# Performance work log

Hardware: AMD Instinct MI355X
Metric: run time of the kernel (lower is better)

## Reference

```python
import jax, jax.numpy as jnp
import numpy as np

D = 2048        # input_size / model dim
H = 2816        # hidden_size per expert (GLU -> w1 has 2*H rows)
E = 8           # num_experts
M = 4096        # tokens (batch*seq)


def setup_inputs() -> dict:
    key = jax.random.key(0)
    k1, k2, k3, k4, k5 = jax.random.split(key, 5)
    x = jax.random.normal(k1, (M, D), dtype=jnp.float32)
    # ParallelExperts init: uniform(-1/fan_in_dim, 1/fan_in_dim); scale kept simple here
    w1 = jax.random.uniform(k2, (E, 2 * H, D), dtype=jnp.float32, minval=-1.0, maxval=1.0) / (2 * H)
    w2 = jax.random.uniform(k3, (E, D, H), dtype=jnp.float32, minval=-1.0, maxval=1.0) / D
    router_w = jax.random.normal(k4, (E, D), dtype=jnp.float32) * (1.0 / np.sqrt(D))
    bias = jnp.zeros((D,), dtype=jnp.float32)
    return {"x": x, "w1": w1, "w2": w2, "router_w": router_w, "bias": bias, "top_k": 2}


def _moe_forward(x, w1, w2, router_w, bias, top_k):
    # Router: logits -> softmax (fp32) -> top-k -> renormalize (fused_moe semantics)
    logits = x @ router_w.T                                # [M, E]
    probs = jax.nn.softmax(logits.astype(jnp.float32), axis=-1)
    topk_w, topk_ids = jax.lax.top_k(probs, top_k)         # [M, k]
    topk_w = topk_w / jnp.sum(topk_w, axis=-1, keepdims=True)
    # Dense combine weights [M, E]: gate weight if expert selected, else 0
    m = x.shape[0]
    combine = jnp.zeros((m, w1.shape[0]), dtype=x.dtype)
    combine = combine.at[jnp.arange(m)[:, None], topk_ids].add(topk_w.astype(x.dtype))
    # Grouped expert GEMMs, expressed as a loop over the small fixed expert set.
    # Contribution of expert e is masked by combine[:, e] (zero for unrouted tokens).
    y = jnp.zeros_like(x)
    hdim = w2.shape[2]
    for e in range(w1.shape[0]):
        g = x @ w1[e].T                                    # [M, 2H]
        h = jax.nn.silu(g[:, :hdim]) * g[:, hdim:]          # silu_and_mul (GLU)
        y = y + combine[:, e:e + 1] * (h @ w2[e].T)         # [M, D]
    return y + bias


def reference(x, w1, w2, router_w, bias, top_k):
    return _moe_forward(x, w1, w2, router_w, bias, top_k)
```

## Files before the change

kernel.cpp:

```cpp
#include <hip/hip_runtime.h>
#include <hip/hip_bf16.h>
#include <stdint.h>

#define M_TOK 4096
#define DDIM  2048
#define HDIM  2816
#define NEXP  8
#define PMAX  9216
#define MAXTILES 72
#define NT1   44
#define NT2   16
#define KT1   32
#define KT2   44

typedef __attribute__((ext_vector_type(8))) short short8;
typedef __attribute__((ext_vector_type(4))) float f32x4;

#define GLD16(g, l) __builtin_amdgcn_global_load_lds(                              \
    (const __attribute__((address_space(1))) unsigned int*)(g),                    \
    (__attribute__((address_space(3))) unsigned int*)(l), 16, 0, 0)

__device__ __forceinline__ unsigned short f2bf(float f) {
  unsigned int u = __float_as_uint(f);
  u += 0x7fffu + ((u >> 16) & 1u);
  return (unsigned short)(u >> 16);
}

__device__ __forceinline__ short8 ldsfrag(const unsigned short* base, int r, int kk) {
  int b = (r << 7) + (kk << 1);
  b ^= (r & 7) << 4;
  return *(const short8*)((const char*)base + b);
}

__global__ void cvt_bf16_k(const float4* __restrict__ in, ushort4* __restrict__ out, int n4) {
  int stride = gridDim.x * blockDim.x;
  for (int i = blockIdx.x * blockDim.x + threadIdx.x; i < n4; i += stride) {
    float4 v = in[i];
    ushort4 o;
    o.x = f2bf(v.x); o.y = f2bf(v.y); o.z = f2bf(v.z); o.w = f2bf(v.w);
    out[i] = o;
  }
}

__global__ void init_k(int* __restrict__ tok, int* __restrict__ counts, int* __restrict__ cursors) {
  int i = blockIdx.x * blockDim.x + threadIdx.x;
  if (i < PMAX) tok[i] = -1;
  if (i < NEXP) { counts[i] = 0; cursors[i] = 0; }
}

__global__ __launch_bounds__(256) void router_k(const float* __restrict__ x,
                                                const float* __restrict__ rw,
                                                float* __restrict__ wgt,
                                                int* __restrict__ eid,
                                                int* __restrict__ counts) {
  int lane = threadIdx.x & 63;
  int wv = threadIdx.x >> 6;
  int t = blockIdx.x * 4 + wv;
  const float* xr = x + (size_t)t * DDIM;
  float acc[NEXP];
#pragma unroll
  for (int e = 0; e < NEXP; ++e) acc[e] = 0.f;
  for (int j = 0; j < DDIM / 64; ++j) {
    float xv = xr[lane + j * 64];
#pragma unroll
    for (int e = 0; e < NEXP; ++e) acc[e] += xv * rw[e * DDIM + lane + j * 64];
  }
#pragma unroll
  for (int e = 0; e < NEXP; ++e) {
#pragma unroll
    for (int s = 32; s > 0; s >>= 1) acc[e] += __shfl_xor(acc[e], s, 64);
  }
  if (lane == 0) {
    float mx = acc[0];
#pragma unroll
    for (int e = 1; e < NEXP; ++e) mx = fmaxf(mx, acc[e]);
    float p[NEXP];
#pragma unroll
    for (int e = 0; e < NEXP; ++e) p[e] = expf(acc[e] - mx);
    int e0 = 0; float p0 = p[0];
#pragma unroll
    for (int e = 1; e < NEXP; ++e) if (p[e] > p0) { p0 = p[e]; e0 = e; }
    int e1 = -1; float p1 = -1.f;
#pragma unroll
    for (int e = 0; e < NEXP; ++e) if (e != e0 && p[e] > p1) { p1 = p[e]; e1 = e; }
    float s = p0 + p1;
    wgt[2 * t] = p0 / s; wgt[2 * t + 1] = p1 / s;
    eid[2 * t] = e0;     eid[2 * t + 1] = e1;
    atomicAdd(&counts[e0], 1);
    atomicAdd(&counts[e1], 1);
  }
}

__global__ void offsets_k(const int* __restrict__ counts, int* __restrict__ offs,
                          int* __restrict__ tile2exp, int* __restrict__ tilerow,
                          int* __restrict__ ntiles) {
  if (threadIdx.x == 0 && blockIdx.x == 0) {
    int o = 0, nt = 0;
    for (int e = 0; e < NEXP; ++e) {
      offs[e] = o;
      int c = counts[e];
      int pt = (c + 127) >> 7;
      for (int i = 0; i < pt; ++i) { tile2exp[nt] = e; tilerow[nt] = o + i * 128; ++nt; }
      o += pt << 7;
    }
    offs[NEXP] = o;
    ntiles[0] = nt;
  }
}

__global__ void scatter_k(const int* __restrict__ eid, const int* __restrict__ offs,
                          int* __restrict__ cursors, int* __restrict__ tok,
                          int* __restrict__ slot) {
  int t = blockIdx.x * blockDim.x + threadIdx.x;
  if (t >= M_TOK) return;
#pragma unroll
  for (int k = 0; k < 2; ++k) {
    int e = eid[2 * t + k];
    int p = offs[e] + atomicAdd(&cursors[e], 1);
    tok[p] = t;
    slot[2 * t + k] = p;
  }
}

__global__ __launch_bounds__(256) void gemm1_k(const unsigned short* __restrict__ xb,
                                               const unsigned short* __restrict__ w1b,
                                               const int* __restrict__ tok,
                                               const int* __restrict__ tile2exp,
                                               const int* __restrict__ tilerow,
                                               const int* __restrict__ ntiles,
                                               unsigned short* __restrict__ h) {
  __shared__ unsigned short lA[128 * 64];
  __shared__ unsigned short lBg[64 * 64];
  __shared__ unsigned short lBu[64 * 64];
  int mt = blockIdx.x;
  if (mt >= ntiles[0]) return;
  int e  = tile2exp[mt];
  int r0 = tilerow[mt];
  int n0 = blockIdx.y * 64;
  int tid = threadIdx.x;
  int lane = tid & 63, wv = tid >> 6;

  int srow = tid >> 3;
  int g16 = (tid & 7) ^ (srow & 7);
  const char* aptr[4];
#pragma unroll
  for (int i = 0; i < 4; ++i) {
    int p = r0 + i * 32 + srow;
    int t = tok[p]; if (t < 0) t = 0;
    aptr[i] = (const char*)xb + ((size_t)t * DDIM + (size_t)g16 * 8) * 2;
  }
  const char* bgptr[2]; const char* buptr[2];
#pragma unroll
  for (int i = 0; i < 2; ++i) {
    size_t rg = (size_t)e * (2 * HDIM) + n0 + i * 32 + srow;
    bgptr[i] = (const char*)w1b + (rg * DDIM + (size_t)g16 * 8) * 2;
    buptr[i] = (const char*)w1b + ((rg + HDIM) * DDIM + (size_t)g16 * 8) * 2;
  }
  char* ldA  = (char*)lA  + tid * 16;
  char* ldBg = (char*)lBg + tid * 16;
  char* ldBu = (char*)lBu + tid * 16;

  f32x4 accg[4][2], accu[4][2];
#pragma unroll
  for (int i = 0; i < 4; ++i)
#pragma unroll
    for (int j = 0; j < 2; ++j) { accg[i][j] = (f32x4)(0.f); accu[i][j] = (f32x4)(0.f); }

  int row0w = (wv >> 1) * 64, col0w = (wv & 1) * 32;
  int l15 = lane & 15, kq = (lane >> 4) * 8;

  for (int kt = 0; kt < KT1; ++kt) {
    __syncthreads();
    int kb = kt * 128;
#pragma unroll
    for (int i = 0; i < 4; ++i) GLD16(aptr[i] + kb, ldA + i * 4096);
#pragma unroll
    for (int i = 0; i < 2; ++i) { GLD16(bgptr[i] + kb, ldBg + i * 4096); GLD16(buptr[i] + kb, ldBu + i * 4096); }
    __syncthreads();
#pragma unroll
    for (int ks = 0; ks < 2; ++ks) {
      int kk = ks * 32 + kq;
      short8 a[4], bg[2], bu[2];
#pragma unroll
      for (int i = 0; i < 4; ++i) a[i] = ldsfrag(lA, row0w + i * 16 + l15, kk);
#pragma unroll
      for (int i = 0; i < 2; ++i) {
        bg[i] = ldsfrag(lBg, col0w + i * 16 + l15, kk);
        bu[i] = ldsfrag(lBu, col0w + i * 16 + l15, kk);
      }
#pragma unroll
      for (int mi = 0; mi < 4; ++mi)
#pragma unroll
        for (int ni = 0; ni < 2; ++ni) {
          accg[mi][ni] = __builtin_amdgcn_mfma_f32_16x16x32_bf16(a[mi], bg[ni], accg[mi][ni], 0, 0, 0);
          accu[mi][ni] = __builtin_amdgcn_mfma_f32_16x16x32_bf16(a[mi], bu[ni], accu[mi][ni], 0, 0, 0);
        }
    }
  }
  int rbase = (lane >> 4) * 4;
#pragma unroll
  for (int mi = 0; mi < 4; ++mi)
#pragma unroll
    for (int ni = 0; ni < 2; ++ni)
#pragma unroll
      for (int j = 0; j < 4; ++j) {
        int rr = row0w + mi * 16 + rbase + j;
        int cc = col0w + ni * 16 + l15;
        float g = accg[mi][ni][j], u = accu[mi][ni][j];
        float sv = g / (1.f + expf(-g));
        h[(size_t)(r0 + rr) * HDIM + n0 + cc] = f2bf(sv * u);
      }
}

__global__ __launch_bounds__(256) void gemm2_k(const unsigned short* __restrict__ h,
                                               const unsigned short* __restrict__ w2b,
                                               const int* __restrict__ tile2exp,
                                               const int* __restrict__ tilerow,
                                               const int* __restrict__ ntiles,
                                               float* __restrict__ yp) {
  __shared__ unsigned short lA[128 * 64];
  __shared__ unsigned short lB[128 * 64];
  int mt = blockIdx.x;
  if (mt >= ntiles[0]) return;
  int e  = tile2exp[mt];
  int r0 = tilerow[mt];
  int n0 = blockIdx.y * 128;
  int tid = threadIdx.x;
  int lane = tid & 63, wv = tid >> 6;

  int srow = tid >> 3;
  int g16 = (tid & 7) ^ (srow & 7);
  const char* aptr[4]; const char* bptr[4];
#pragma unroll
  for (int i = 0; i < 4; ++i) {
    aptr[i] = (const char*)h + ((size_t)(r0 + i * 32 + srow) * HDIM + (size_t)g16 * 8) * 2;
    bptr[i] = (const char*)w2b + (((size_t)e * DDIM + n0 + i * 32 + srow) * HDIM + (size_t)g16 * 8) * 2;
  }
  char* ldA = (char*)lA + tid * 16;
  char* ldB = (char*)lB + tid * 16;

  f32x4 acc[4][4];
#pragma unroll
  for (int i = 0; i < 4; ++i)
#pragma unroll
    for (int j = 0; j < 4; ++j) acc[i][j] = (f32x4)(0.f);

  int row0w = (wv >> 1) * 64, col0w = (wv & 1) * 64;
  int l15 = lane & 15, kq = (lane >> 4) * 8;

  for (int kt = 0; kt < KT2; ++kt) {
    __syncthreads();
    int kb = kt * 128;
#pragma unroll
    for (int i = 0; i < 4; ++i) { GLD16(aptr[i] + kb, ldA + i * 4096); GLD16(bptr[i] + kb, ldB + i * 4096); }
    __syncthreads();
#pragma unroll
    for (int ks = 0; ks < 2; ++ks) {
      int kk = ks * 32 + kq;
      short8 a[4], b[4];
#pragma unroll
      for (int i = 0; i < 4; ++i) a[i] = ldsfrag(lA, row0w + i * 16 + l15, kk);
#pragma unroll
      for (int i = 0; i < 4; ++i) b[i] = ldsfrag(lB, col0w + i * 16 + l15, kk);
#pragma unroll
      for (int mi = 0; mi < 4; ++mi)
#pragma unroll
        for (int ni = 0; ni < 4; ++ni)
          acc[mi][ni] = __builtin_amdgcn_mfma_f32_16x16x32_bf16(a[mi], b[ni], acc[mi][ni], 0, 0, 0);
    }
  }
  int rbase = (lane >> 4) * 4;
#pragma unroll
  for (int mi = 0; mi < 4; ++mi)
#pragma unroll
    for (int ni = 0; ni < 4; ++ni)
#pragma unroll
      for (int j = 0; j < 4; ++j) {
        int rr = row0w + mi * 16 + rbase + j;
        int cc = col0w + ni * 16 + l15;
        yp[(size_t)(r0 + rr) * DDIM + n0 + cc] = acc[mi][ni][j];
      }
}

__global__ void combine_k(const float* __restrict__ yp, const float* __restrict__ wgt,
                          const int* __restrict__ slot, const float* __restrict__ bias,
                          float* __restrict__ out) {
  int idx = blockIdx.x * blockDim.x + threadIdx.x;
  int t = idx >> 9, q = idx & 511;
  float w0 = wgt[2 * t], w1 = wgt[2 * t + 1];
  int s0 = slot[2 * t], s1 = slot[2 * t + 1];
  float4 av = ((const float4*)(yp + (size_t)s0 * DDIM))[q];
  float4 bv = ((const float4*)(yp + (size_t)s1 * DDIM))[q];
  float4 bi = ((const float4*)bias)[q];
  float4 o;
  o.x = w0 * av.x + w1 * bv.x + bi.x;
  o.y = w0 * av.y + w1 * bv.y + bi.y;
  o.z = w0 * av.z + w1 * bv.z + bi.z;
  o.w = w0 * av.w + w1 * bv.w + bi.w;
  ((float4*)out)[idx] = o;
}

extern "C" void kernel_launch(void* const* d_in, const int* in_sizes, int n_in,
                              void* d_out, int out_size, void* d_ws, size_t ws_size,
                              hipStream_t stream) {
  const float* x    = (const float*)d_in[0];
  const float* w1   = (const float*)d_in[1];
  const float* w2   = (const float*)d_in[2];
  const float* rw   = (const float*)d_in[3];
  const float* bias = (const float*)d_in[4];
  float* out = (float*)d_out;

  char* ws = (char*)d_ws;
  size_t off = 0;
  auto alloc = [&](size_t bytes) -> void* {
    void* p = ws + off;
    off = (off + bytes + 255) & ~(size_t)255;
    return p;
  };
  unsigned short* w1b = (unsigned short*)alloc((size_t)NEXP * 2 * HDIM * DDIM * 2);
  unsigned short* w2b = (unsigned short*)alloc((size_t)NEXP * DDIM * HDIM * 2);
  unsigned short* xb  = (unsigned short*)alloc((size_t)M_TOK * DDIM * 2);
  unsigned short* h   = (unsigned short*)alloc((size_t)PMAX * HDIM * 2);
  float* yp           = (float*)alloc((size_t)PMAX * DDIM * 4);
  float* wgt          = (float*)alloc((size_t)M_TOK * 2 * 4);
  int* eid            = (int*)alloc((size_t)M_TOK * 2 * 4);
  int* slot           = (int*)alloc((size_t)M_TOK * 2 * 4);
  int* tok            = (int*)alloc((size_t)PMAX * 4);
  int* counts         = (int*)alloc(64 * 4);
  int* cursors        = (int*)alloc(64 * 4);
  int* offs           = (int*)alloc(64 * 4);
  int* ntiles         = (int*)alloc(64 * 4);
  int* tile2exp       = (int*)alloc(128 * 4);
  int* tilerow        = (int*)alloc(128 * 4);

  hipLaunchKernelGGL(init_k, dim3((PMAX + 255) / 256), dim3(256), 0, stream, tok, counts, cursors);
  hipLaunchKernelGGL(cvt_bf16_k, dim3(2048), dim3(256), 0, stream,
                     (const float4*)w1, (ushort4*)w1b, (int)((size_t)NEXP * 2 * HDIM * DDIM / 4));
  hipLaunchKernelGGL(cvt_bf16_k, dim3(2048), dim3(256), 0, stream,
                     (const float4*)w2, (ushort4*)w2b, (int)((size_t)NEXP * DDIM * HDIM / 4));
  hipLaunchKernelGGL(cvt_bf16_k, dim3(2048), dim3(256), 0, stream,
                     (const float4*)x, (ushort4*)xb, (int)((size_t)M_TOK * DDIM / 4));
  hipLaunchKernelGGL(router_k, dim3(M_TOK / 4), dim3(256), 0, stream, x, rw, wgt, eid, counts);
  hipLaunchKernelGGL(offsets_k, dim3(1), dim3(64), 0, stream, counts, offs, tile2exp, tilerow, ntiles);
  hipLaunchKernelGGL(scatter_k, dim3((M_TOK + 255) / 256), dim3(256), 0, stream, eid, offs, cursors, tok, slot);
  hipLaunchKernelGGL(gemm1_k, dim3(MAXTILES, NT1), dim3(256), 0, stream, xb, w1b, tok, tile2exp, tilerow, ntiles, h);
  hipLaunchKernelGGL(gemm2_k, dim3(MAXTILES, NT2), dim3(256), 0, stream, h, w2b, tile2exp, tilerow, ntiles, yp);
  hipLaunchKernelGGL(combine_k, dim3(M_TOK * (DDIM / 4) / 256), dim3(256), 0, stream, yp, wgt, slot, bias, out);
}
```

Before: 834.9 us.

## Rewrite expert GEMMs with 256-row tiles and 4-stage async LDS pipeline

Both grouped GEMMs move to 256-row by 128/256-column tiles with 512 threads, a 4-deep ring of global-to-LDS buffers, and explicit vmcnt waits, so loads overlap MFMA work in place of the old load-then-sync loop. Expert groups are padded to 256 rows. The gate/up product in gemm1 now uses one tile whose halves are exchanged through LDS. The gemm2 partial output is stored as bf16 to cut write and read traffic in combine. The risks are more padding waste, 128KB of LDS per block limiting occupancy, and reduced output precision.

```diff
diff --git a/kernel.cpp b/kernel.cpp
--- a/kernel.cpp
+++ b/kernel.cpp
@@ -6,12 +6,12 @@
 #define DDIM  2048
 #define HDIM  2816
 #define NEXP  8
-#define PMAX  9216
-#define MAXTILES 72
-#define NT1   44
-#define NT2   16
-#define KT1   32
-#define KT2   44
+#define PMAX  10240
+#define MAXTILES 40
+#define NB1   22
+#define NB2   8
+#define NT1   64
+#define NT2   88
 
 typedef __attribute__((ext_vector_type(8))) short short8;
 typedef __attribute__((ext_vector_type(4))) float f32x4;
@@ -19,18 +19,48 @@
 #define GLD16(g, l) __builtin_amdgcn_global_load_lds(                              \
     (const __attribute__((address_space(1))) unsigned int*)(g),                    \
     (__attribute__((address_space(3))) unsigned int*)(l), 16, 0, 0)
+
+#define VMCNT(n) asm volatile("s_waitcnt vmcnt(" #n ")" ::: "memory")
 
 __device__ __forceinline__ unsigned short f2bf(float f) {
   unsigned int u = __float_as_uint(f);
   u += 0x7fffu + ((u >> 16) & 1u);
   return (unsigned short)(u >> 16);
 }
-
-__device__ __forceinline__ short8 ldsfrag(const unsigned short* base, int r, int kk) {
-  int b = (r << 7) + (kk << 1);
-  b ^= (r & 7) << 4;
-  return *(const short8*)((const char*)base + b);
-}
+__device__ __forceinline__ float bf2f(unsigned short u) {
+  return __uint_as_float(((unsigned)u) << 16);
+}
+
+#define PHASE(TT, VM, STG)                                                       \
+  {                                                                              \
+    VMCNT(VM);                                                                   \
+    __builtin_amdgcn_s_barrier();                                                \
+    asm volatile("" ::: "memory");                                               \
+    if (STG) {                                                                   \
+      int st_ = (TT) + 3;                                                        \
+      int t4s_ = st_ & 3;                                                        \
+      size_t kb_ = (size_t)st_ * 64;                                             \
+      GLD16(aS0 + kb_, ldsp + t4s_ * 16384 + aD0);                               \
+      GLD16(aS1 + kb_, ldsp + t4s_ * 16384 + aD1);                               \
+      GLD16(bS0 + kb_, ldsp + 65536 + t4s_ * 16384 + aD0);                       \
+      GLD16(bS1 + kb_, ldsp + 65536 + t4s_ * 16384 + aD1);                       \
+    }                                                                            \
+    {                                                                            \
+      int t4_ = (TT) & 3;                                                        \
+      const char* ab_ = ldsp + t4_ * 16384;                                      \
+      const char* bb_ = ldsp + 65536 + t4_ * 16384;                              \
+      short8 av_[8], bv_[4];                                                     \
+      _Pragma("unroll") for (int mi = 0; mi < 8; ++mi)                           \
+        av_[mi] = *(const short8*)(ab_ + aoff[mi]);                              \
+      _Pragma("unroll") for (int ni = 0; ni < 4; ++ni)                           \
+        bv_[ni] = *(const short8*)(bb_ + boff[ni]);                              \
+      __builtin_amdgcn_s_setprio(1);                                             \
+      _Pragma("unroll") for (int mi = 0; mi < 8; ++mi)                           \
+        _Pragma("unroll") for (int ni = 0; ni < 4; ++ni)                         \
+          acc[mi][ni] = __builtin_amdgcn_mfma_f32_16x16x32_bf16(av_[mi], bv_[ni], acc[mi][ni], 0, 0, 0); \
+      __builtin_amdgcn_s_setprio(0);                                             \
+    }                                                                            \
+  }
 
 __global__ void cvt_bf16_k(const float4* __restrict__ in, ushort4* __restrict__ out, int n4) {
   int stride = gridDim.x * blockDim.x;
@@ -99,9 +129,9 @@
     for (int e = 0; e < NEXP; ++e) {
       offs[e] = o;
       int c = counts[e];
-      int pt = (c + 127) >> 7;
-      for (int i = 0; i < pt; ++i) { tile2exp[nt] = e; tilerow[nt] = o + i * 128; ++nt; }
-      o += pt << 7;
+      int pt = (c + 255) >> 8;
+      for (int i = 0; i < pt; ++i) { tile2exp[nt] = e; tilerow[nt] = o + i * 256; ++nt; }
+      o += pt << 8;
     }
     offs[NEXP] = o;
     ntiles[0] = nt;
@@ -122,182 +152,188 @@
   }
 }
 
-__global__ __launch_bounds__(256) void gemm1_k(const unsigned short* __restrict__ xb,
-                                               const unsigned short* __restrict__ w1b,
-                                               const int* __restrict__ tok,
-                                               const int* __restrict__ tile2exp,
-                                               const int* __restrict__ tilerow,
-                                               const int* __restrict__ ntiles,
-                                               unsigned short* __restrict__ h) {
-  __shared__ unsigned short lA[128 * 64];
-  __shared__ unsigned short lBg[64 * 64];
-  __shared__ unsigned short lBu[64 * 64];
+__global__ __launch_bounds__(512, 2) void gemm1_k(const unsigned short* __restrict__ xb,
+                                                  const unsigned short* __restrict__ w1b,
+                                                  const int* __restrict__ tok,
+                                                  const int* __restrict__ tile2exp,
+                                                  const int* __restrict__ tilerow,
+                                                  const int* __restrict__ ntiles,
+                                                  unsigned short* __restrict__ h) {
+  __shared__ char ldsp[131072];
   int mt = blockIdx.x;
   if (mt >= ntiles[0]) return;
-  int e  = tile2exp[mt];
-  int r0 = tilerow[mt];
-  int n0 = blockIdx.y * 64;
-  int tid = threadIdx.x;
-  int lane = tid & 63, wv = tid >> 6;
-
-  int srow = tid >> 3;
-  int g16 = (tid & 7) ^ (srow & 7);
-  const char* aptr[4];
-#pragma unroll
-  for (int i = 0; i < 4; ++i) {
-    int p = r0 + i * 32 + srow;
-    int t = tok[p]; if (t < 0) t = 0;
-    aptr[i] = (const char*)xb + ((size_t)t * DDIM + (size_t)g16 * 8) * 2;
-  }
-  const char* bgptr[2]; const char* buptr[2];
-#pragma unroll
-  for (int i = 0; i < 2; ++i) {
-    size_t rg = (size_t)e * (2 * HDIM) + n0 + i * 32 + srow;
-    bgptr[i] = (const char*)w1b + (rg * DDIM + (size_t)g16 * 8) * 2;
-    buptr[i] = (const char*)w1b + ((rg + HDIM) * DDIM + (size_t)g16 * 8) * 2;
-  }
-  char* ldA  = (char*)lA  + tid * 16;
-  char* ldBg = (char*)lBg + tid * 16;
-  char* ldBu = (char*)lBu + tid * 16;
-
-  f32x4 accg[4][2], accu[4][2];
-#pragma unroll
-  for (int i = 0; i < 4; ++i)
-#pragma unroll
-    for (int j = 0; j < 2; ++j) { accg[i][j] = (f32x4)(0.f); accu[i][j] = (f32x4)(0.f); }
-
-  int row0w = (wv >> 1) * 64, col0w = (wv & 1) * 32;
-  int l15 = lane & 15, kq = (lane >> 4) * 8;
-
-  for (int kt = 0; kt < KT1; ++kt) {
-    __syncthreads();
-    int kb = kt * 128;
-#pragma unroll
-    for (int i = 0; i < 4; ++i) GLD16(aptr[i] + kb, ldA + i * 4096);
-#pragma unroll
-    for (int i = 0; i < 2; ++i) { GLD16(bgptr[i] + kb, ldBg + i * 4096); GLD16(buptr[i] + kb, ldBu + i * 4096); }
-    __syncthreads();
-#pragma unroll
-    for (int ks = 0; ks < 2; ++ks) {
-      int kk = ks * 32 + kq;
-      short8 a[4], bg[2], bu[2];
-#pragma unroll
-      for (int i = 0; i < 4; ++i) a[i] = ldsfrag(lA, row0w + i * 16 + l15, kk);
-#pragma unroll
-      for (int i = 0; i < 2; ++i) {
-        bg[i] = ldsfrag(lBg, col0w + i * 16 + l15, kk);
-        bu[i] = ldsfrag(lBu, col0w + i * 16 + l15, kk);
-      }
-#pragma unroll
-      for (int mi = 0; mi < 4; ++mi)
-#pragma unroll
-        for (int ni = 0; ni < 2; ++ni) {
-          accg[mi][ni] = __builtin_amdgcn_mfma_f32_16x16x32_bf16(a[mi], bg[ni], accg[mi][ni], 0, 0, 0);
-          accu[mi][ni] = __builtin_amdgcn_mfma_f32_16x16x32_bf16(a[mi], bu[ni], accu[mi][ni], 0, 0, 0);
+  int e = tile2exp[mt], r0 = tilerow[mt];
+  int n0 = blockIdx.y * 128;
+  int tid = threadIdx.x, lane = tid & 63;
+  int wv = tid >> 6, wm = wv >> 2, wn = wv & 3;
+  int l15 = lane & 15, g = lane >> 4;
+
+  int row0 = tid >> 2, g0 = (tid & 3) ^ ((row0 >> 1) & 3);
+  int s1i = 512 + tid;
+  int row1 = s1i >> 2, g1 = (s1i & 3) ^ ((row1 >> 1) & 3);
+  int t0 = tok[r0 + row0]; if (t0 < 0) t0 = 0;
+  int t1 = tok[r0 + row1]; if (t1 < 0) t1 = 0;
+  const char* aS0 = (const char*)xb + (size_t)t0 * (DDIM * 2) + g0 * 16;
+  const char* aS1 = (const char*)xb + (size_t)t1 * (DDIM * 2) + g1 * 16;
+  size_t w1r0 = (size_t)e * (2 * HDIM) +
+                (row0 < 128 ? (size_t)(n0 + row0) : (size_t)(HDIM + n0 + row0 - 128));
+  size_t w1r1 = (size_t)e * (2 * HDIM) +
+                (row1 < 128 ? (size_t)(n0 + row1) : (size_t)(HDIM + n0 + row1 - 128));
+  const char* bS0 = (const char*)w1b + w1r0 * (DDIM * 2) + g0 * 16;
+  const char* bS1 = (const char*)w1b + w1r1 * (DDIM * 2) + g1 * 16;
+  int aD0 = tid * 16, aD1 = 8192 + tid * 16;
+
+  int aoff[8], boff[4];
+#pragma unroll
+  for (int mi = 0; mi < 8; ++mi) {
+    int r = wm * 128 + mi * 16 + l15;
+    aoff[mi] = r * 64 + ((g ^ ((r >> 1) & 3)) * 16);
+  }
+#pragma unroll
+  for (int ni = 0; ni < 4; ++ni) {
+    int r = wn * 64 + ni * 16 + l15;
+    boff[ni] = r * 64 + ((g ^ ((r >> 1) & 3)) * 16);
+  }
+
+  f32x4 acc[8][4];
+#pragma unroll
+  for (int mi = 0; mi < 8; ++mi)
+#pragma unroll
+    for (int ni = 0; ni < 4; ++ni) acc[mi][ni] = (f32x4)(0.f);
+
+#pragma unroll
+  for (int t = 0; t < 3; ++t) {
+    GLD16(aS0 + (size_t)t * 64, ldsp + t * 16384 + aD0);
+    GLD16(aS1 + (size_t)t * 64, ldsp + t * 16384 + aD1);
+    GLD16(bS0 + (size_t)t * 64, ldsp + 65536 + t * 16384 + aD0);
+    GLD16(bS1 + (size_t)t * 64, ldsp + 65536 + t * 16384 + aD1);
+  }
+
+  int T = 0;
+  for (; T + 3 < NT1; ++T) PHASE(T, 8, 1);
+  PHASE(T, 8, 0); ++T;
+  PHASE(T, 4, 0); ++T;
+  PHASE(T, 0, 0);
+
+  __syncthreads();
+  float* xch = (float*)ldsp;
+  int rbase = (lane >> 4) * 4;
+  if (wn >= 2) {
+    int uc0 = (wn - 2) * 64;
+#pragma unroll
+    for (int mi = 0; mi < 8; ++mi)
+#pragma unroll
+      for (int ni = 0; ni < 4; ++ni)
+#pragma unroll
+        for (int j = 0; j < 4; ++j) {
+          int r = wm * 128 + mi * 16 + rbase + j;
+          int c = uc0 + ni * 16 + l15;
+          xch[r * 128 + c] = acc[mi][ni][j];
         }
-    }
-  }
-  int rbase = (lane >> 4) * 4;
-#pragma unroll
-  for (int mi = 0; mi < 4; ++mi)
-#pragma unroll
-    for (int ni = 0; ni < 2; ++ni)
-#pragma unroll
-      for (int j = 0; j < 4; ++j) {
-        int rr = row0w + mi * 16 + rbase + j;
-        int cc = col0w + ni * 16 + l15;
-        float g = accg[mi][ni][j], u = accu[mi][ni][j];
-        float sv = g / (1.f + expf(-g));
-        h[(size_t)(r0 + rr) * HDIM + n0 + cc] = f2bf(sv * u);
-      }
-}
-
-__global__ __launch_bounds__(256) void gemm2_k(const unsigned short* __restrict__ h,
-                                               const unsigned short* __restrict__ w2b,
-                                               const int* __restrict__ tile2exp,
-                                               const int* __restrict__ tilerow,
-                                               const int* __restrict__ ntiles,
-                                               float* __restrict__ yp) {
-  __shared__ unsigned short lA[128 * 64];
-  __shared__ unsigned short lB[128 * 64];
+  }
+  __syncthreads();
+  if (wn < 2) {
+#pragma unroll
+    for (int mi = 0; mi < 8; ++mi)
+#pragma unroll
+      for (int ni = 0; ni < 4; ++ni)
+#pragma unroll
+        for (int j = 0; j < 4; ++j) {
+          int r = wm * 128 + mi * 16 + rbase + j;
+          int c = wn * 64 + ni * 16 + l15;
+          float gg = acc[mi][ni][j];
+          float u = xch[r * 128 + c];
+          float sv = gg / (1.f + expf(-gg));
+          h[(size_t)(r0 + r) * HDIM + n0 + c] = f2bf(sv * u);
+        }
+  }
+}
+
+__global__ __launch_bounds__(512, 2) void gemm2_k(const unsigned short* __restrict__ h,
+                                                  const unsigned short* __restrict__ w2b,
+                                                  const int* __restrict__ tile2exp,
+                                                  const int* __restrict__ tilerow,
+                                                  const int* __restrict__ ntiles,
+                                                  unsigned short* __restrict__ yp) {
+  __shared__ char ldsp[131072];
   int mt = blockIdx.x;
   if (mt >= ntiles[0]) return;
-  int e  = tile2exp[mt];
-  int r0 = tilerow[mt];
-  int n0 = blockIdx.y * 128;
-  int tid = threadIdx.x;
-  int lane = tid & 63, wv = tid >> 6;
-
-  int srow = tid >> 3;
-  int g16 = (tid & 7) ^ (srow & 7);
-  const char* aptr[4]; const char* bptr[4];
-#pragma unroll
-  for (int i = 0; i < 4; ++i) {
-    aptr[i] = (const char*)h + ((size_t)(r0 + i * 32 + srow) * HDIM + (size_t)g16 * 8) * 2;
-    bptr[i] = (const char*)w2b + (((size_t)e * DDIM + n0 + i * 32 + srow) * HDIM + (size_t)g16 * 8) * 2;
-  }
-  char* ldA = (char*)lA + tid * 16;
-  char* ldB = (char*)lB + tid * 16;
-
-  f32x4 acc[4][4];
-#pragma unroll
-  for (int i = 0; i < 4; ++i)
-#pragma unroll
-    for (int j = 0; j < 4; ++j) acc[i][j] = (f32x4)(0.f);
-
-  int row0w = (wv >> 1) * 64, col0w = (wv & 1) * 64;
-  int l15 = lane & 15, kq = (lane >> 4) * 8;
-
-  for (int kt = 0; kt < KT2; ++kt) {
-    __syncthreads();
-    int kb = kt * 128;
-#pragma unroll
-    for (int i = 0; i < 4; ++i) { GLD16(aptr[i] + kb, ldA + i * 4096); GLD16(bptr[i] + kb, ldB + i * 4096); }
-    __syncthreads();
-#pragma unroll
-    for (int ks = 0; ks < 2; ++ks) {
-      int kk = ks * 32 + kq;
-      short8 a[4], b[4];
-#pragma unroll
-      for (int i = 0; i < 4; ++i) a[i] = ldsfrag(lA, row0w + i * 16 + l15, kk);
-#pragma unroll
-      for (int i = 0; i < 4; ++i) b[i] = ldsfrag(lB, col0w + i * 16 + l15, kk);
-#pragma unroll
-      for (int mi = 0; mi < 4; ++mi)
-#pragma unroll
-        for (int ni = 0; ni < 4; ++ni)
-          acc[mi][ni] = __builtin_amdgcn_mfma_f32_16x16x32_bf16(a[mi], b[ni], acc[mi][ni], 0, 0, 0);
-    }
-  }
+  int e = tile2exp[mt], r0 = tilerow[mt];
+  int n0 = blockIdx.y * 256;
+  int tid = threadIdx.x, lane = tid & 63;
+  int wv = tid >> 6, wm = wv >> 2, wn = wv & 3;
+  int l15 = lane & 15, g = lane >> 4;
+
+  int row0 = tid >> 2, g0 = (tid & 3) ^ ((row0 >> 1) & 3);
+  int s1i = 512 + tid;
+  int row1 = s1i >> 2, g1 = (s1i & 3) ^ ((row1 >> 1) & 3);
+  const char* aS0 = (const char*)h + (size_t)(r0 + row0) * (HDIM * 2) + g0 * 16;
+  const char* aS1 = (const char*)h + (size_t)(r0 + row1) * (HDIM * 2) + g1 * 16;
+  const char* bS0 = (const char*)w2b + ((size_t)e * DDIM + n0 + row0) * (HDIM * 2) + g0 * 16;
+  const char* bS1 = (const char*)w2b + ((size_t)e * DDIM + n0 + row1) * (HDIM * 2) + g1 * 16;
+  int aD0 = tid * 16, aD1 = 8192 + tid * 16;
+
+  int aoff[8], boff[4];
+#pragma unroll
+  for (int mi = 0; mi < 8; ++mi) {
+    int r = wm * 128 + mi * 16 + l15;
+    aoff[mi] = r * 64 + ((g ^ ((r >> 1) & 3)) * 16);
+  }
+#pragma unroll
+  for (int ni = 0; ni < 4; ++ni) {
+    int r = wn * 64 + ni * 16 + l15;
+    boff[ni] = r * 64 + ((g ^ ((r >> 1) & 3)) * 16);
+  }
+
+  f32x4 acc[8][4];
+#pragma unroll
+  for (int mi = 0; mi < 8; ++mi)
+#pragma unroll
+    for (int ni = 0; ni < 4; ++ni) acc[mi][ni] = (f32x4)(0.f);
+
+#pragma unroll
+  for (int t = 0; t < 3; ++t) {
+    GLD16(aS0 + (size_t)t * 64, ldsp + t * 16384 + aD0);
+    GLD16(aS1 + (size_t)t * 64, ldsp + t * 16384 + aD1);
+    GLD16(bS0 + (size_t)t * 64, ldsp + 65536 + t * 16384 + aD0);
+    GLD16(bS1 + (size_t)t * 64, ldsp + 65536 + t * 16384 + aD1);
+  }
+
+  int T = 0;
+  for (; T + 3 < NT2; ++T) PHASE(T, 8, 1);
+  PHASE(T, 8, 0); ++T;
+  PHASE(T, 4, 0); ++T;
+  PHASE(T, 0, 0);
+
   int rbase = (lane >> 4) * 4;
 #pragma unroll
-  for (int mi = 0; mi < 4; ++mi)
+  for (int mi = 0; mi < 8; ++mi)
 #pragma unroll
     for (int ni = 0; ni < 4; ++ni)
 #pragma unroll
       for (int j = 0; j < 4; ++j) {
-        int rr = row0w + mi * 16 + rbase + j;
-        int cc = col0w + ni * 16 + l15;
-        yp[(size_t)(r0 + rr) * DDIM + n0 + cc] = acc[mi][ni][j];
+        int r = r0 + wm * 128 + mi * 16 + rbase + j;
+        int c = n0 + wn * 64 + ni * 16 + l15;
+        yp[(size_t)r * DDIM + c] = f2bf(acc[mi][ni][j]);
       }
 }
 
-__global__ void combine_k(const float* __restrict__ yp, const float* __restrict__ wgt,
+__global__ void combine_k(const unsigned short* __restrict__ yp, const float* __restrict__ wgt,
                           const int* __restrict__ slot, const float* __restrict__ bias,
                           float* __restrict__ out) {
   int idx = blockIdx.x * blockDim.x + threadIdx.x;
-  int t = idx >> 9, q = idx & 511;
+  int t = idx >> 8, q = (idx & 255) * 8;
   float w0 = wgt[2 * t], w1 = wgt[2 * t + 1];
   int s0 = slot[2 * t], s1 = slot[2 * t + 1];
-  float4 av = ((const float4*)(yp + (size_t)s0 * DDIM))[q];
-  float4 bv = ((const float4*)(yp + (size_t)s1 * DDIM))[q];
-  float4 bi = ((const float4*)bias)[q];
-  float4 o;
-  o.x = w0 * av.x + w1 * bv.x + bi.x;
-  o.y = w0 * av.y + w1 * bv.y + bi.y;
-  o.z = w0 * av.z + w1 * bv.z + bi.z;
-  o.w = w0 * av.w + w1 * bv.w + bi.w;
-  ((float4*)out)[idx] = o;
+  short8 a8 = *(const short8*)(yp + (size_t)s0 * DDIM + q);
+  short8 b8 = *(const short8*)(yp + (size_t)s1 * DDIM + q);
+  float* op = out + (size_t)t * DDIM + q;
+#pragma unroll
+  for (int k = 0; k < 8; ++k) {
+    float av = bf2f((unsigned short)a8[k]);
+    float bv = bf2f((unsigned short)b8[k]);
+    op[k] = w0 * av + w1 * bv + bias[q + k];
+  }
 }
 
 extern "C" void kernel_launch(void* const* d_in, const int* in_sizes, int n_in,
@@ -321,7 +357,7 @@
   unsigned short* w2b = (unsigned short*)alloc((size_t)NEXP * DDIM * HDIM * 2);
   unsigned short* xb  = (unsigned short*)alloc((size_t)M_TOK * DDIM * 2);
   unsigned short* h   = (unsigned short*)alloc((size_t)PMAX * HDIM * 2);
-  float* yp           = (float*)alloc((size_t)PMAX * DDIM * 4);
+  unsigned short* yp  = (unsigned short*)alloc((size_t)PMAX * DDIM * 2);
   float* wgt          = (float*)alloc((size_t)M_TOK * 2 * 4);
   int* eid            = (int*)alloc((size_t)M_TOK * 2 * 4);
   int* slot           = (int*)alloc((size_t)M_TOK * 2 * 4);
@@ -343,7 +379,7 @@
   hipLaunchKernelGGL(router_k, dim3(M_TOK / 4), dim3(256), 0, stream, x, rw, wgt, eid, counts);
   hipLaunchKernelGGL(offsets_k, dim3(1), dim3(64), 0, stream, counts, offs, tile2exp, tilerow, ntiles);
   hipLaunchKernelGGL(scatter_k, dim3((M_TOK + 255) / 256), dim3(256), 0, stream, eid, offs, cursors, tok, slot);
-  hipLaunchKernelGGL(gemm1_k, dim3(MAXTILES, NT1), dim3(256), 0, stream, xb, w1b, tok, tile2exp, tilerow, ntiles, h);
-  hipLaunchKernelGGL(gemm2_k, dim3(MAXTILES, NT2), dim3(256), 0, stream, h, w2b, tile2exp, tilerow, ntiles, yp);
-  hipLaunchKernelGGL(combine_k, dim3(M_TOK * (DDIM / 4) / 256), dim3(256), 0, stream, yp, wgt, slot, bias, out);
-}
+  hipLaunchKernelGGL(gemm1_k, dim3(MAXTILES, NB1), dim3(512), 0, stream, xb, w1b, tok, tile2exp, tilerow, ntiles, h);
+  hipLaunchKernelGGL(gemm2_k, dim3(MAXTILES, NB2), dim3(512), 0, stream, h, w2b, tile2exp, tilerow, ntiles, yp);
+  hipLaunchKernelGGL(combine_k, dim3(M_TOK * (DDIM / 8) / 256), dim3(256), 0, stream, yp, wgt, slot, bias, out);
+}
```

Result: faster. 763.5 us (-8.6%).
